# Kernel tuning notes

Hardware: AMD Instinct MI355X
Metric: run time of the kernel (lower is better)

Reference implementation:

```python
import jax, jax.numpy as jnp
import numpy as np

N = 100000      # nodes
E = 1600000     # edges
G = 1024        # graphs in batch
BASE = 1000     # baseline (TF-IDF) dim
AUG = 384       # augmented (LM) dim
H = 256         # hidden dim
C = 2           # classes
EPS = 1e-5      # BatchNorm eps


def setup_inputs() -> dict:
    key = jax.random.key(0)
    ks = jax.random.split(key, 10)
    x = jax.random.normal(ks[0], (N, BASE), jnp.float32)
    x_aug = jax.random.normal(ks[1], (N, AUG), jnp.float32)
    edge_index = jax.random.randint(ks[2], (2, E), 0, N)
    batch = jnp.sort(jax.random.randint(ks[3], (N,), 0, G))

    def lin(k, fin, fout):
        return (jax.random.normal(k, (fin, fout), jnp.float32) / np.sqrt(fin)).astype(jnp.float32)

    return dict(
        x=x, x_aug=x_aug,
        fusion_W=lin(ks[4], BASE + AUG, H), fusion_b=jnp.zeros((H,), jnp.float32),
        W0=lin(ks[5], H, H), b0=jnp.zeros((H,), jnp.float32),
        g0=jnp.ones((H,), jnp.float32), be0=jnp.zeros((H,), jnp.float32),
        W1=lin(ks[6], H, H), b1=jnp.zeros((H,), jnp.float32),
        g1=jnp.ones((H,), jnp.float32), be1=jnp.zeros((H,), jnp.float32),
        fc_W=lin(ks[7], H, C), fc_b=jnp.zeros((C,), jnp.float32),
        edge_index=edge_index, batch=batch,
    )


def _gcn(h, W, b, src, dst, dinv):
    # PyG GCNConv: x' = D^{-1/2}(A+I)D^{-1/2} (x W) + b, self-loop weight 1
    h = h @ W                                     # [N, H]
    norm = dinv[src] * dinv[dst]                  # [E]
    agg = jax.ops.segment_sum(h[src] * norm[:, None], dst, num_segments=N)
    agg = agg + h * (dinv * dinv)[:, None]        # self-loop term
    return agg + b


def _bn(x, gamma, beta):
    # training-mode BatchNorm1d (batch statistics, biased variance)
    m = x.mean(axis=0)
    v = x.var(axis=0)
    return (x - m) * jax.lax.rsqrt(v + EPS) * gamma + beta


def reference(x, x_aug, fusion_W, fusion_b, W0, b0, g0, be0, W1, b1, g1, be1,
              fc_W, fc_b, edge_index, batch):
    src, dst = edge_index[0], edge_index[1]
    # degrees with self-loops (edge weight 1), scattered at destination
    deg = jnp.zeros((N,), x.dtype).at[dst].add(1.0) + 1.0
    dinv = jax.lax.rsqrt(deg)

    # feature fusion ('concat'): Linear(baseline+aug -> hidden) + ReLU
    h = jax.nn.relu(jnp.concatenate([x, x_aug], axis=1) @ fusion_W + fusion_b)

    # GCN layer 1 + BN + ReLU (dropout is identity in eval)
    h = jax.nn.relu(_bn(_gcn(h, W0, b0, src, dst, dinv), g0, be0))
    # GCN layer 2 + BN + ReLU
    h = jax.nn.relu(_bn(_gcn(h, W1, b1, src, dst, dinv), g1, be1))

    # global mean pool over graphs
    cnt = jax.ops.segment_sum(jnp.ones((N,), h.dtype), batch, num_segments=G)
    pooled = jax.ops.segment_sum(h, batch, num_segments=G) / jnp.maximum(cnt, 1.0)[:, None]

    logits = pooled @ fc_W + fc_b                 # [G, C]
    return jax.nn.log_softmax(logits, axis=1)
```

## Files before the change

### kernel.cpp

```cpp
#include <hip/hip_runtime.h>
#include <hip/hip_bf16.h>

#define N_NODES 100000
#define N_EDGES 1600000
#define N_GRAPH 1024
#define DIM_BASE 1000
#define DIM_AUG 384
#define DIM_IN 1384
#define KPAD_IN 1408
#define HD 256
#define BN_EPS 1e-5f

typedef _Float16 f16x8 __attribute__((ext_vector_type(8)));
typedef _Float16 f16x4 __attribute__((ext_vector_type(4)));
typedef float f32x4 __attribute__((ext_vector_type(4)));

__global__ void zero_kernel(unsigned int* __restrict__ p, int n) {
    int i = blockIdx.x * blockDim.x + threadIdx.x;
    if (i < n) p[i] = 0u;
}

__global__ void count_edges_kernel(const int* __restrict__ dst, int* __restrict__ counts, int e) {
    int i = blockIdx.x * blockDim.x + threadIdx.x;
    if (i < e) atomicAdd(&counts[dst[i]], 1);
}

__global__ __launch_bounds__(256) void deg_bsum_kernel(const int* __restrict__ counts,
                                                       int* __restrict__ bsum, int n) {
    __shared__ int sh[256];
    int t = threadIdx.x;
    int base = blockIdx.x * 1024 + t * 4;
    int s = 0;
    if (base < n) {
        int4 v = *(const int4*)&counts[base];
        s = v.x + v.y + v.z + v.w;
    }
    sh[t] = s;
    __syncthreads();
    for (int off = 128; off > 0; off >>= 1) {
        if (t < off) sh[t] += sh[t + off];
        __syncthreads();
    }
    if (t == 0) bsum[blockIdx.x] = sh[0];
}

__global__ __launch_bounds__(128) void scan_bsum_kernel(const int* __restrict__ bsum,
                                                        int* __restrict__ boff, int nb) {
    __shared__ int sh[128];
    int t = threadIdx.x;
    int v = (t < nb) ? bsum[t] : 0;
    sh[t] = v;
    __syncthreads();
    for (int off = 1; off < 128; off <<= 1) {
        int u = (t >= off) ? sh[t - off] : 0;
        __syncthreads();
        sh[t] += u;
        __syncthreads();
    }
    if (t < nb) boff[t] = sh[t] - v;
}

__global__ __launch_bounds__(256) void emit_csr_kernel(const int* __restrict__ counts,
                                                       const int* __restrict__ boff,
                                                       int* __restrict__ row_ptr,
                                                       int* __restrict__ cursor,
                                                       float* __restrict__ dinv, int n, int etot) {
    __shared__ int sh[256];
    int t = threadIdx.x;
    int base = blockIdx.x * 1024 + t * 4;
    int c0 = 0, c1 = 0, c2 = 0, c3 = 0;
    if (base < n) {
        int4 v = *(const int4*)&counts[base];
        c0 = v.x; c1 = v.y; c2 = v.z; c3 = v.w;
    }
    int s = c0 + c1 + c2 + c3;
    sh[t] = s;
    __syncthreads();
    for (int off = 1; off < 256; off <<= 1) {
        int u = (t >= off) ? sh[t - off] : 0;
        __syncthreads();
        sh[t] += u;
        __syncthreads();
    }
    if (base < n) {
        int run = boff[blockIdx.x] + sh[t] - s;
        int4 rp;
        rp.x = run; run += c0;
        rp.y = run; run += c1;
        rp.z = run; run += c2;
        rp.w = run;
        *(int4*)&row_ptr[base] = rp;
        *(int4*)&cursor[base] = rp;
        float4 dv;
        dv.x = rsqrtf((float)c0 + 1.0f);
        dv.y = rsqrtf((float)c1 + 1.0f);
        dv.z = rsqrtf((float)c2 + 1.0f);
        dv.w = rsqrtf((float)c3 + 1.0f);
        *(float4*)&dinv[base] = dv;
    }
    if (blockIdx.x == 0 && t == 0) row_ptr[n] = etot;
}

__global__ void fill_edges_kernel(const int* __restrict__ src, const int* __restrict__ dst,
                                  int* __restrict__ cursor, int* __restrict__ col, int e) {
    int i = blockIdx.x * blockDim.x + threadIdx.x;
    if (i < e) {
        int pos = atomicAdd(&cursor[dst[i]], 1);
        col[pos] = src[i];
    }
}

__global__ __launch_bounds__(256) void btrans_kernel(const float* __restrict__ W,
                                                     f16x8* __restrict__ Bt,
                                                     int K, int nchunks) {
    int idx = blockIdx.x * 256 + threadIdx.x;
    if (idx >= nchunks) return;
    int col = idx & 255;
    int kbase = (idx >> 8) * 8;
    f16x8 h;
#pragma unroll
    for (int j = 0; j < 8; ++j) {
        int k = kbase + j;
        float v = (k < K) ? W[(size_t)k * HD + col] : 0.f;
        h[j] = (_Float16)v;
    }
    Bt[idx] = h;
}

__global__ __launch_bounds__(512, 4) void fusion_mfma_kernel(
        const float* __restrict__ x, const float* __restrict__ xa,
        const f16x8* __restrict__ Bt, const float* __restrict__ bias,
        _Float16* __restrict__ C, int M) {
    __shared__ _Float16 Al[2][128 * 40];
    int tid = threadIdx.x;
    int lane = tid & 63;
    int wid = tid >> 6;
    int wr = wid >> 2, wc = wid & 3;
    int l16 = lane & 15, l4 = lane >> 4;
    int row0 = blockIdx.x * 128;

    f32x4 acc[4][4];
#pragma unroll
    for (int m = 0; m < 4; ++m)
#pragma unroll
        for (int n = 0; n < 4; ++n) acc[m][n] = (f32x4){0.f, 0.f, 0.f, 0.f};

    int arow = tid >> 2;
    int akq = (tid & 3) * 8;
    int ar = row0 + arow;
    int arc = (ar < M) ? ar : (M - 1);

    auto loadA = [&](int s, float* fv) {
        int kg = s * 32 + akq;
        if (kg < DIM_IN) {
            const float* sp = (kg < DIM_BASE) ? (x + (size_t)arc * DIM_BASE + kg)
                                              : (xa + (size_t)arc * DIM_AUG + (kg - DIM_BASE));
            float4 v0 = ((const float4*)sp)[0];
            float4 v1 = ((const float4*)sp)[1];
            fv[0] = v0.x; fv[1] = v0.y; fv[2] = v0.z; fv[3] = v0.w;
            fv[4] = v1.x; fv[5] = v1.y; fv[6] = v1.z; fv[7] = v1.w;
        } else {
#pragma unroll
            for (int j = 0; j < 8; ++j) fv[j] = 0.f;
        }
    };

    const int S = KPAD_IN / 32;
    float fv0[8], fv1[8];
    loadA(0, fv0);
    loadA(1, fv1);

    int bcol = wc * 64 + l16;

    auto iter = [&](int s, float* fv) {
        int buf = s & 1;
        f16x8 av;
#pragma unroll
        for (int j = 0; j < 8; ++j) av[j] = (_Float16)fv[j];
        *(f16x8*)&Al[buf][arow * 40 + akq] = av;
        if (s + 2 < S) loadA(s + 2, fv);
        __syncthreads();
        f16x8 bf[4];
#pragma unroll
        for (int n = 0; n < 4; ++n)
            bf[n] = Bt[(size_t)(s * 4 + l4) * 256 + bcol + n * 16];
#pragma unroll
        for (int m = 0; m < 4; ++m) {
            f16x8 af = *(const f16x8*)&Al[buf][(wr * 64 + m * 16 + l16) * 40 + l4 * 8];
#pragma unroll
            for (int n = 0; n < 4; ++n)
                acc[m][n] = __builtin_amdgcn_mfma_f32_16x16x32_f16(af, bf[n], acc[m][n], 0, 0, 0);
        }
    };

    for (int s = 0; s < S; s += 2) {
        iter(s, fv0);
        iter(s + 1, fv1);
    }

#pragma unroll
    for (int n = 0; n < 4; ++n) {
        int colF = wc * 64 + n * 16 + l16;
        float bc = bias[colF];
#pragma unroll
        for (int m = 0; m < 4; ++m) {
#pragma unroll
            for (int r = 0; r < 4; ++r) {
                int rowF = row0 + wr * 64 + m * 16 + l4 * 4 + r;
                if (rowF < M)
                    C[(size_t)rowF * HD + colF] = (_Float16)fmaxf(acc[m][n][r] + bc, 0.f);
            }
        }
    }
}

__global__ __launch_bounds__(512, 4) void hgemm_f16_kernel(
        const _Float16* __restrict__ A, const f16x8* __restrict__ Bt,
        _Float16* __restrict__ C, int M) {
    __shared__ _Float16 Al[2][128 * 40];
    int tid = threadIdx.x;
    int lane = tid & 63;
    int wid = tid >> 6;
    int wr = wid >> 2, wc = wid & 3;
    int l16 = lane & 15, l4 = lane >> 4;
    int row0 = blockIdx.x * 128;

    f32x4 acc[4][4];
#pragma unroll
    for (int m = 0; m < 4; ++m)
#pragma unroll
        for (int n = 0; n < 4; ++n) acc[m][n] = (f32x4){0.f, 0.f, 0.f, 0.f};

    int arow = tid >> 2;
    int akq = (tid & 3) * 8;
    int ar = row0 + arow;
    int arc = (ar < M) ? ar : (M - 1);
    int bcol = wc * 64 + l16;

    const int S = HD / 32;
    f16x8 av0 = *(const f16x8*)&A[(size_t)arc * HD + akq];
    f16x8 av1 = *(const f16x8*)&A[(size_t)arc * HD + 32 + akq];

    auto iter = [&](int s, f16x8& av) {
        int buf = s & 1;
        *(f16x8*)&Al[buf][arow * 40 + akq] = av;
        if (s + 2 < S) av = *(const f16x8*)&A[(size_t)arc * HD + (s + 2) * 32 + akq];
        __syncthreads();
        f16x8 bf[4];
#pragma unroll
        for (int n = 0; n < 4; ++n)
            bf[n] = Bt[(size_t)(s * 4 + l4) * 256 + bcol + n * 16];
#pragma unroll
        for (int m = 0; m < 4; ++m) {
            f16x8 af = *(const f16x8*)&Al[buf][(wr * 64 + m * 16 + l16) * 40 + l4 * 8];
#pragma unroll
            for (int n = 0; n < 4; ++n)
                acc[m][n] = __builtin_amdgcn_mfma_f32_16x16x32_f16(af, bf[n], acc[m][n], 0, 0, 0);
        }
    };

    for (int s = 0; s < S; s += 2) {
        iter(s, av0);
        iter(s + 1, av1);
    }

#pragma unroll
    for (int n = 0; n < 4; ++n) {
        int colF = wc * 64 + n * 16 + l16;
#pragma unroll
        for (int m = 0; m < 4; ++m) {
#pragma unroll
            for (int r = 0; r < 4; ++r) {
                int rowF = row0 + wr * 64 + m * 16 + l4 * 4 + r;
                if (rowF < M)
                    C[(size_t)rowF * HD + colF] = (_Float16)acc[m][n][r];
            }
        }
    }
}

__global__ __launch_bounds__(512, 4) void hgemm_bn_kernel(
        const float* __restrict__ A, const f16x8* __restrict__ Bt,
        const float* __restrict__ bnp, _Float16* __restrict__ C, int M) {
    __shared__ _Float16 Al[2][128 * 40];
    __shared__ float bns[512];
    int tid = threadIdx.x;
    int lane = tid & 63;
    int wid = tid >> 6;
    int wr = wid >> 2, wc = wid & 3;
    int l16 = lane & 15, l4 = lane >> 4;
    int row0 = blockIdx.x * 128;

    bns[tid] = bnp[tid];
    __syncthreads();

    f32x4 acc[4][4];
#pragma unroll
    for (int m = 0; m < 4; ++m)
#pragma unroll
        for (int n = 0; n < 4; ++n) acc[m][n] = (f32x4){0.f, 0.f, 0.f, 0.f};

    int arow = tid >> 2;
    int akq = (tid & 3) * 8;
    int ar = row0 + arow;
    int arc = (ar < M) ? ar : (M - 1);
    int bcol = wc * 64 + l16;

    auto loadA = [&](int s, float* fv) {
        const float* sp = A + (size_t)arc * HD + s * 32 + akq;
        float4 v0 = ((const float4*)sp)[0];
        float4 v1 = ((const float4*)sp)[1];
        fv[0] = v0.x; fv[1] = v0.y; fv[2] = v0.z; fv[3] = v0.w;
        fv[4] = v1.x; fv[5] = v1.y; fv[6] = v1.z; fv[7] = v1.w;
    };

    const int S = HD / 32;
    float fv0[8], fv1[8];
    loadA(0, fv0);
    loadA(1, fv1);

    auto iter = [&](int s, float* fv) {
        int buf = s & 1;
        int kg = s * 32 + akq;
        f16x8 av;
#pragma unroll
        for (int j = 0; j < 8; ++j)
            av[j] = (_Float16)fmaxf(fmaf(fv[j], bns[kg + j], bns[HD + kg + j]), 0.f);
        *(f16x8*)&Al[buf][arow * 40 + akq] = av;
        if (s + 2 < S) loadA(s + 2, fv);
        __syncthreads();
        f16x8 bf[4];
#pragma unroll
        for (int n = 0; n < 4; ++n)
            bf[n] = Bt[(size_t)(s * 4 + l4) * 256 + bcol + n * 16];
#pragma unroll
        for (int m = 0; m < 4; ++m) {
            f16x8 af = *(const f16x8*)&Al[buf][(wr * 64 + m * 16 + l16) * 40 + l4 * 8];
#pragma unroll
            for (int n = 0; n < 4; ++n)
                acc[m][n] = __builtin_amdgcn_mfma_f32_16x16x32_f16(af, bf[n], acc[m][n], 0, 0, 0);
        }
    };

    for (int s = 0; s < S; s += 2) {
        iter(s, fv0);
        iter(s + 1, fv1);
    }

#pragma unroll
    for (int n = 0; n < 4; ++n) {
        int colF = wc * 64 + n * 16 + l16;
#pragma unroll
        for (int m = 0; m < 4; ++m) {
#pragma unroll
            for (int r = 0; r < 4; ++r) {
                int rowF = row0 + wr * 64 + m * 16 + l4 * 4 + r;
                if (rowF < M)
                    C[(size_t)rowF * HD + colF] = (_Float16)acc[m][n][r];
            }
        }
    }
}

__global__ __launch_bounds__(256) void agg_kernel(
        const _Float16* __restrict__ t, const float* __restrict__ dinv,
        const int* __restrict__ row_ptr, const int* __restrict__ col,
        const float* __restrict__ bias, float* __restrict__ outp, int n) {
    int wid = threadIdx.x >> 6;
    int lane = threadIdx.x & 63;
    int i = blockIdx.x * 4 + wid;
    if (i >= n) return;
    int c0 = lane * 4;
    float di = dinv[i];
    float di2 = di * di;
    f16x4 sv = *(const f16x4*)&t[(size_t)i * HD + c0];
    float a0 = (float)sv[0] * di2, a1 = (float)sv[1] * di2;
    float a2 = (float)sv[2] * di2, a3 = (float)sv[3] * di2;
    int e = row_ptr[i], end = row_ptr[i + 1];
    for (; e + 1 < end; e += 2) {
        int s0 = col[e], s1 = col[e + 1];
        float w0 = dinv[s0] * di, w1 = dinv[s1] * di;
        f16x4 v0 = *(const f16x4*)&t[(size_t)s0 * HD + c0];
        f16x4 v1 = *(const f16x4*)&t[(size_t)s1 * HD + c0];
        a0 = fmaf((float)v0[0], w0, a0); a1 = fmaf((float)v0[1], w0, a1);
        a2 = fmaf((float)v0[2], w0, a2); a3 = fmaf((float)v0[3], w0, a3);
        a0 = fmaf((float)v1[0], w1, a0); a1 = fmaf((float)v1[1], w1, a1);
        a2 = fmaf((float)v1[2], w1, a2); a3 = fmaf((float)v1[3], w1, a3);
    }
    if (e < end) {
        int s0 = col[e];
        float w0 = dinv[s0] * di;
        f16x4 v0 = *(const f16x4*)&t[(size_t)s0 * HD + c0];
        a0 = fmaf((float)v0[0], w0, a0); a1 = fmaf((float)v0[1], w0, a1);
        a2 = fmaf((float)v0[2], w0, a2); a3 = fmaf((float)v0[3], w0, a3);
    }
    float4 b = *(const float4*)&bias[c0];
    float4 o;
    o.x = a0 + b.x; o.y = a1 + b.y; o.z = a2 + b.z; o.w = a3 + b.w;
    *(float4*)&outp[(size_t)i * HD + c0] = o;
}

__global__ __launch_bounds__(256) void bn_stats_kernel(const float* __restrict__ a,
                                                       float* __restrict__ sums, int n) {
    int tid = threadIdx.x;
    int r0 = blockIdx.x * 256;
    int r1 = min(r0 + 256, n);
    float s = 0.f, s2 = 0.f;
    for (int r = r0; r < r1; ++r) {
        float v = a[(size_t)r * HD + tid];
        s += v;
        s2 = fmaf(v, v, s2);
    }
    atomicAdd(&sums[tid], s);
    atomicAdd(&sums[HD + tid], s2);
}

__global__ __launch_bounds__(256) void bn_final_kernel(const float* __restrict__ sums,
                                                       const float* __restrict__ g,
                                                       const float* __restrict__ be,
                                                       float* __restrict__ p, int n) {
    int tid = threadIdx.x;
    float mean = sums[tid] / (float)n;
    float var = sums[HD + tid] / (float)n - mean * mean;
    float sc = g[tid] * rsqrtf(var + BN_EPS);
    p[tid] = sc;
    p[HD + tid] = be[tid] - mean * sc;
}

__global__ void graph_cnt_kernel(const int* __restrict__ batch, float* __restrict__ cnt, int n) {
    int i = blockIdx.x * blockDim.x + threadIdx.x;
    if (i < n) atomicAdd(&cnt[batch[i]], 1.0f);
}

__global__ __launch_bounds__(256) void bn_relu_pool_kernel(const float* __restrict__ a,
                                                           const float* __restrict__ p,
                                                           const int* __restrict__ batch,
                                                           float* __restrict__ pooled, int n) {
    int tid = threadIdx.x;
    int n0 = blockIdx.x * 64;
    int n1 = min(n0 + 64, n);
    if (n0 >= n) return;
    float sc = p[tid], sh = p[HD + tid];
    int curg = batch[n0];
    float acc = 0.f;
    for (int i = n0; i < n1; ++i) {
        int g = batch[i];
        if (g != curg) {
            atomicAdd(&pooled[(size_t)curg * HD + tid], acc);
            acc = 0.f;
            curg = g;
        }
        acc += fmaxf(fmaf(a[(size_t)i * HD + tid], sc, sh), 0.f);
    }
    atomicAdd(&pooled[(size_t)curg * HD + tid], acc);
}

__global__ __launch_bounds__(64) void head_kernel(const float* __restrict__ pooled,
                                                  const float* __restrict__ cnt,
                                                  const float* __restrict__ fcW,
                                                  const float* __restrict__ fcb,
                                                  float* __restrict__ outp) {
    int g = blockIdx.x, lane = threadIdx.x;
    float inv = 1.0f / fmaxf(cnt[g], 1.0f);
    float a0 = 0.f, a1 = 0.f;
    for (int j = lane; j < HD; j += 64) {
        float v = pooled[(size_t)g * HD + j] * inv;
        a0 = fmaf(v, fcW[j * 2 + 0], a0);
        a1 = fmaf(v, fcW[j * 2 + 1], a1);
    }
    for (int off = 32; off > 0; off >>= 1) {
        a0 += __shfl_down(a0, off);
        a1 += __shfl_down(a1, off);
    }
    if (lane == 0) {
        float l0 = a0 + fcb[0], l1 = a1 + fcb[1];
        float m = fmaxf(l0, l1);
        float lse = m + logf(expf(l0 - m) + expf(l1 - m));
        outp[g * 2 + 0] = l0 - lse;
        outp[g * 2 + 1] = l1 - lse;
    }
}

extern "C" void kernel_launch(void* const* d_in, const int* in_sizes, int n_in,
                              void* d_out, int out_size, void* d_ws, size_t ws_size,
                              hipStream_t stream) {
    const float* x        = (const float*)d_in[0];
    const float* x_aug    = (const float*)d_in[1];
    const float* fusion_W = (const float*)d_in[2];
    const float* fusion_b = (const float*)d_in[3];
    const float* W0       = (const float*)d_in[4];
    const float* b0       = (const float*)d_in[5];
    const float* g0       = (const float*)d_in[6];
    const float* be0      = (const float*)d_in[7];
    const float* W1       = (const float*)d_in[8];
    const float* b1       = (const float*)d_in[9];
    const float* g1       = (const float*)d_in[10];
    const float* be1      = (const float*)d_in[11];
    const float* fc_W     = (const float*)d_in[12];
    const float* fc_b     = (const float*)d_in[13];
    const int*   eidx     = (const int*)d_in[14];
    const int*   batch    = (const int*)d_in[15];
    float* outp = (float*)d_out;

    const int N = N_NODES, E = N_EDGES, G = N_GRAPH;
    const int* src = eidx;
    const int* dst = eidx + E;

    size_t off = 0;
    char* ws = (char*)d_ws;
    auto take = [&](size_t nbytes) -> void* {
        void* p = ws + off;
        off = (off + nbytes + 255) & ~(size_t)255;
        return p;
    };
    float*     bufA    = (float*)take((size_t)N * HD * 4);
    _Float16*  bufH    = (_Float16*)take((size_t)N * HD * 2);
    _Float16*  bufT    = (_Float16*)take((size_t)N * HD * 2);
    float*     dinv    = (float*)take((size_t)N * 4);
    int*       row_ptr = (int*)take((size_t)(N + 1) * 4);
    int*       cursor  = (int*)take((size_t)N * 4);
    int*       col     = (int*)take((size_t)E * 4);
    float*     bn1p    = (float*)take(512 * 4);
    float*     bn2p    = (float*)take(512 * 4);
    int*       bsum    = (int*)take(128 * 4);
    int*       boff    = (int*)take(128 * 4);
    f16x8*     BtF     = (f16x8*)take((size_t)(KPAD_IN / 8) * 256 * 16);
    f16x8*     Bt0     = (f16x8*)take((size_t)(HD / 8) * 256 * 16);
    f16x8*     Bt1     = (f16x8*)take((size_t)(HD / 8) * 256 * 16);
    size_t zwords = (size_t)N + 512 + 512 + (size_t)G * HD + G;
    unsigned int* zbase = (unsigned int*)take(zwords * 4);
    int*   counts = (int*)zbase;
    float* bn1s   = (float*)(zbase + N);
    float* bn2s   = bn1s + 512;
    float* pooled = bn2s + 512;
    float* cnt    = pooled + (size_t)G * HD;

    const int nchF = (KPAD_IN / 8) * 256;
    const int nchH = (HD / 8) * 256;
    const int nScanB = (N + 1023) / 1024;

    zero_kernel<<<(int)((zwords + 255) / 256), 256, 0, stream>>>(zbase, (int)zwords);
    count_edges_kernel<<<(E + 255) / 256, 256, 0, stream>>>(dst, counts, E);
    deg_bsum_kernel<<<nScanB, 256, 0, stream>>>(counts, bsum, N);
    scan_bsum_kernel<<<1, 128, 0, stream>>>(bsum, boff, nScanB);
    emit_csr_kernel<<<nScanB, 256, 0, stream>>>(counts, boff, row_ptr, cursor, dinv, N, E);
    fill_edges_kernel<<<(E + 255) / 256, 256, 0, stream>>>(src, dst, cursor, col, E);
    btrans_kernel<<<(nchF + 255) / 256, 256, 0, stream>>>(fusion_W, BtF, DIM_IN, nchF);
    btrans_kernel<<<(nchH + 255) / 256, 256, 0, stream>>>(W0, Bt0, HD, nchH);
    btrans_kernel<<<(nchH + 255) / 256, 256, 0, stream>>>(W1, Bt1, HD, nchH);

    const int gblocks = (N + 127) / 128;
    fusion_mfma_kernel<<<gblocks, 512, 0, stream>>>(x, x_aug, BtF, fusion_b, bufH, N);
    hgemm_f16_kernel<<<gblocks, 512, 0, stream>>>(bufH, Bt0, bufT, N);
    agg_kernel<<<(N + 3) / 4, 256, 0, stream>>>(bufT, dinv, row_ptr, col, b0, bufA, N);
    bn_stats_kernel<<<(N + 255) / 256, 256, 0, stream>>>(bufA, bn1s, N);
    bn_final_kernel<<<1, 256, 0, stream>>>(bn1s, g0, be0, bn1p, N);
    hgemm_bn_kernel<<<gblocks, 512, 0, stream>>>(bufA, Bt1, bn1p, bufT, N);
    agg_kernel<<<(N + 3) / 4, 256, 0, stream>>>(bufT, dinv, row_ptr, col, b1, bufA, N);
    bn_stats_kernel<<<(N + 255) / 256, 256, 0, stream>>>(bufA, bn2s, N);
    bn_final_kernel<<<1, 256, 0, stream>>>(bn2s, g1, be1, bn2p, N);
    graph_cnt_kernel<<<(N + 255) / 256, 256, 0, stream>>>(batch, cnt, N);
    bn_relu_pool_kernel<<<(N + 63) / 64, 256, 0, stream>>>(bufA, bn2p, batch, pooled, N);
    head_kernel<<<G, 64, 0, stream>>>(pooled, cnt, fc_W, fc_b, outp);
}
```

Measured before the change: 1.017 ms.

## Rework dense GEMMs to register-direct 32x32x16 MFMA without LDS staging

All three dense GEMM kernels (fusion, layer-0, layer-1 with fused BN) drop the shared-memory A staging and __syncthreads. Each wave now owns 32 full rows and loads its A fragments straight from global memory into registers. The kernels also switch from 16x16x32 to 32x32x16 MFMA, covering all 256 output columns per wave with 8 accumulators, and use 256-thread blocks. The aim is to remove LDS round-trips and barrier stalls. The cost is much higher register pressure (128 accumulator floats plus double-buffered B fragments), and B is reloaded per wave with less sharing across waves.

```diff
diff --git a/kernel.cpp b/kernel.cpp
--- a/kernel.cpp
+++ b/kernel.cpp
@@ -14,6 +14,7 @@
 typedef _Float16 f16x8 __attribute__((ext_vector_type(8)));
 typedef _Float16 f16x4 __attribute__((ext_vector_type(4)));
 typedef float f32x4 __attribute__((ext_vector_type(4)));
+typedef float f32x16 __attribute__((ext_vector_type(16)));
 
 __global__ void zero_kernel(unsigned int* __restrict__ p, int n) {
     int i = blockIdx.x * blockDim.x + threadIdx.x;
@@ -127,34 +128,31 @@
     Bt[idx] = h;
 }
 
-__global__ __launch_bounds__(512, 4) void fusion_mfma_kernel(
+
+__global__ __launch_bounds__(256, 2) void fusion_mfma_kernel(
         const float* __restrict__ x, const float* __restrict__ xa,
         const f16x8* __restrict__ Bt, const float* __restrict__ bias,
         _Float16* __restrict__ C, int M) {
-    __shared__ _Float16 Al[2][128 * 40];
     int tid = threadIdx.x;
     int lane = tid & 63;
     int wid = tid >> 6;
-    int wr = wid >> 2, wc = wid & 3;
-    int l16 = lane & 15, l4 = lane >> 4;
-    int row0 = blockIdx.x * 128;
-
-    f32x4 acc[4][4];
-#pragma unroll
-    for (int m = 0; m < 4; ++m)
-#pragma unroll
-        for (int n = 0; n < 4; ++n) acc[m][n] = (f32x4){0.f, 0.f, 0.f, 0.f};
-
-    int arow = tid >> 2;
-    int akq = (tid & 3) * 8;
-    int ar = row0 + arow;
-    int arc = (ar < M) ? ar : (M - 1);
+    int l31 = lane & 31;
+    int lhi = lane >> 5;
+    int row = blockIdx.x * 128 + wid * 32 + l31;
+    int rowc = (row < M) ? row : (M - 1);
+    const float* xr = x + (size_t)rowc * DIM_BASE;
+    const float* xar = xa + (size_t)rowc * DIM_AUG;
+
+    f32x16 acc[8];
+#pragma unroll
+    for (int nf = 0; nf < 8; ++nf)
+#pragma unroll
+        for (int e = 0; e < 16; ++e) acc[nf][e] = 0.f;
 
     auto loadA = [&](int s, float* fv) {
-        int kg = s * 32 + akq;
+        int kg = s * 16 + lhi * 8;
         if (kg < DIM_IN) {
-            const float* sp = (kg < DIM_BASE) ? (x + (size_t)arc * DIM_BASE + kg)
-                                              : (xa + (size_t)arc * DIM_AUG + (kg - DIM_BASE));
+            const float* sp = (kg < DIM_BASE) ? (xr + kg) : (xar + (kg - DIM_BASE));
             float4 v0 = ((const float4*)sp)[0];
             float4 v1 = ((const float4*)sp)[1];
             fv[0] = v0.x; fv[1] = v0.y; fv[2] = v0.z; fv[3] = v0.w;
@@ -164,200 +162,188 @@
             for (int j = 0; j < 8; ++j) fv[j] = 0.f;
         }
     };
-
-    const int S = KPAD_IN / 32;
+    auto loadB = [&](int s, f16x8* bq) {
+        const f16x8* bp = Bt + (size_t)(s * 2 + lhi) * 256 + l31;
+#pragma unroll
+        for (int nf = 0; nf < 8; ++nf) bq[nf] = bp[nf * 32];
+    };
+
+    const int S = KPAD_IN / 16;
     float fv0[8], fv1[8];
+    f16x8 bq0[8], bq1[8];
     loadA(0, fv0);
     loadA(1, fv1);
-
-    int bcol = wc * 64 + l16;
-
-    auto iter = [&](int s, float* fv) {
-        int buf = s & 1;
-        f16x8 av;
-#pragma unroll
-        for (int j = 0; j < 8; ++j) av[j] = (_Float16)fv[j];
-        *(f16x8*)&Al[buf][arow * 40 + akq] = av;
-        if (s + 2 < S) loadA(s + 2, fv);
-        __syncthreads();
-        f16x8 bf[4];
-#pragma unroll
-        for (int n = 0; n < 4; ++n)
-            bf[n] = Bt[(size_t)(s * 4 + l4) * 256 + bcol + n * 16];
-#pragma unroll
-        for (int m = 0; m < 4; ++m) {
-            f16x8 af = *(const f16x8*)&Al[buf][(wr * 64 + m * 16 + l16) * 40 + l4 * 8];
-#pragma unroll
-            for (int n = 0; n < 4; ++n)
-                acc[m][n] = __builtin_amdgcn_mfma_f32_16x16x32_f16(af, bf[n], acc[m][n], 0, 0, 0);
+    loadB(0, bq0);
+
+    for (int s = 0; s < S; s += 2) {
+        f16x8 a0;
+#pragma unroll
+        for (int j = 0; j < 8; ++j) a0[j] = (_Float16)fv0[j];
+        if (s + 2 < S) loadA(s + 2, fv0);
+        loadB(s + 1, bq1);
+#pragma unroll
+        for (int nf = 0; nf < 8; ++nf)
+            acc[nf] = __builtin_amdgcn_mfma_f32_32x32x16_f16(a0, bq0[nf], acc[nf], 0, 0, 0);
+
+        f16x8 a1;
+#pragma unroll
+        for (int j = 0; j < 8; ++j) a1[j] = (_Float16)fv1[j];
+        if (s + 3 < S) loadA(s + 3, fv1);
+        if (s + 2 < S) loadB(s + 2, bq0);
+#pragma unroll
+        for (int nf = 0; nf < 8; ++nf)
+            acc[nf] = __builtin_amdgcn_mfma_f32_32x32x16_f16(a1, bq1[nf], acc[nf], 0, 0, 0);
+    }
+
+    int rbase = blockIdx.x * 128 + wid * 32 + 4 * lhi;
+#pragma unroll
+    for (int nf = 0; nf < 8; ++nf) {
+        int colF = nf * 32 + l31;
+        float bc = bias[colF];
+#pragma unroll
+        for (int r = 0; r < 16; ++r) {
+            int rowF = rbase + (r & 3) + 8 * (r >> 2);
+            if (rowF < M)
+                C[(size_t)rowF * HD + colF] = (_Float16)fmaxf(acc[nf][r] + bc, 0.f);
         }
-    };
-
-    for (int s = 0; s < S; s += 2) {
-        iter(s, fv0);
-        iter(s + 1, fv1);
-    }
-
-#pragma unroll
-    for (int n = 0; n < 4; ++n) {
-        int colF = wc * 64 + n * 16 + l16;
-        float bc = bias[colF];
-#pragma unroll
-        for (int m = 0; m < 4; ++m) {
-#pragma unroll
-            for (int r = 0; r < 4; ++r) {
-                int rowF = row0 + wr * 64 + m * 16 + l4 * 4 + r;
-                if (rowF < M)
-                    C[(size_t)rowF * HD + colF] = (_Float16)fmaxf(acc[m][n][r] + bc, 0.f);
-            }
-        }
-    }
-}
-
-__global__ __launch_bounds__(512, 4) void hgemm_f16_kernel(
+    }
+}
+
+__global__ __launch_bounds__(256, 2) void hgemm_f16_kernel(
         const _Float16* __restrict__ A, const f16x8* __restrict__ Bt,
         _Float16* __restrict__ C, int M) {
-    __shared__ _Float16 Al[2][128 * 40];
     int tid = threadIdx.x;
     int lane = tid & 63;
     int wid = tid >> 6;
-    int wr = wid >> 2, wc = wid & 3;
-    int l16 = lane & 15, l4 = lane >> 4;
-    int row0 = blockIdx.x * 128;
-
-    f32x4 acc[4][4];
-#pragma unroll
-    for (int m = 0; m < 4; ++m)
-#pragma unroll
-        for (int n = 0; n < 4; ++n) acc[m][n] = (f32x4){0.f, 0.f, 0.f, 0.f};
-
-    int arow = tid >> 2;
-    int akq = (tid & 3) * 8;
-    int ar = row0 + arow;
-    int arc = (ar < M) ? ar : (M - 1);
-    int bcol = wc * 64 + l16;
-
-    const int S = HD / 32;
-    f16x8 av0 = *(const f16x8*)&A[(size_t)arc * HD + akq];
-    f16x8 av1 = *(const f16x8*)&A[(size_t)arc * HD + 32 + akq];
-
-    auto iter = [&](int s, f16x8& av) {
-        int buf = s & 1;
-        *(f16x8*)&Al[buf][arow * 40 + akq] = av;
-        if (s + 2 < S) av = *(const f16x8*)&A[(size_t)arc * HD + (s + 2) * 32 + akq];
-        __syncthreads();
-        f16x8 bf[4];
-#pragma unroll
-        for (int n = 0; n < 4; ++n)
-            bf[n] = Bt[(size_t)(s * 4 + l4) * 256 + bcol + n * 16];
-#pragma unroll
-        for (int m = 0; m < 4; ++m) {
-            f16x8 af = *(const f16x8*)&Al[buf][(wr * 64 + m * 16 + l16) * 40 + l4 * 8];
-#pragma unroll
-            for (int n = 0; n < 4; ++n)
-                acc[m][n] = __builtin_amdgcn_mfma_f32_16x16x32_f16(af, bf[n], acc[m][n], 0, 0, 0);
+    int l31 = lane & 31;
+    int lhi = lane >> 5;
+    int row = blockIdx.x * 128 + wid * 32 + l31;
+    int rowc = (row < M) ? row : (M - 1);
+    const _Float16* ar = A + (size_t)rowc * HD + lhi * 8;
+
+    f32x16 acc[8];
+#pragma unroll
+    for (int nf = 0; nf < 8; ++nf)
+#pragma unroll
+        for (int e = 0; e < 16; ++e) acc[nf][e] = 0.f;
+
+    auto loadB = [&](int s, f16x8* bq) {
+        const f16x8* bp = Bt + (size_t)(s * 2 + lhi) * 256 + l31;
+#pragma unroll
+        for (int nf = 0; nf < 8; ++nf) bq[nf] = bp[nf * 32];
+    };
+
+    const int S = HD / 16;
+    f16x8 a0 = *(const f16x8*)(ar + 0 * 16);
+    f16x8 a1 = *(const f16x8*)(ar + 1 * 16);
+    f16x8 bq0[8], bq1[8];
+    loadB(0, bq0);
+
+    for (int s = 0; s < S; s += 2) {
+        f16x8 ac = a0;
+        if (s + 2 < S) a0 = *(const f16x8*)(ar + (s + 2) * 16);
+        loadB(s + 1, bq1);
+#pragma unroll
+        for (int nf = 0; nf < 8; ++nf)
+            acc[nf] = __builtin_amdgcn_mfma_f32_32x32x16_f16(ac, bq0[nf], acc[nf], 0, 0, 0);
+
+        f16x8 ad = a1;
+        if (s + 3 < S) a1 = *(const f16x8*)(ar + (s + 3) * 16);
+        if (s + 2 < S) loadB(s + 2, bq0);
+#pragma unroll
+        for (int nf = 0; nf < 8; ++nf)
+            acc[nf] = __builtin_amdgcn_mfma_f32_32x32x16_f16(ad, bq1[nf], acc[nf], 0, 0, 0);
+    }
+
+    int rbase = blockIdx.x * 128 + wid * 32 + 4 * lhi;
+#pragma unroll
+    for (int nf = 0; nf < 8; ++nf) {
+        int colF = nf * 32 + l31;
+#pragma unroll
+        for (int r = 0; r < 16; ++r) {
+            int rowF = rbase + (r & 3) + 8 * (r >> 2);
+            if (rowF < M)
+                C[(size_t)rowF * HD + colF] = (_Float16)acc[nf][r];
         }
-    };
-
-    for (int s = 0; s < S; s += 2) {
-        iter(s, av0);
-        iter(s + 1, av1);
-    }
-
-#pragma unroll
-    for (int n = 0; n < 4; ++n) {
-        int colF = wc * 64 + n * 16 + l16;
-#pragma unroll
-        for (int m = 0; m < 4; ++m) {
-#pragma unroll
-            for (int r = 0; r < 4; ++r) {
-                int rowF = row0 + wr * 64 + m * 16 + l4 * 4 + r;
-                if (rowF < M)
-                    C[(size_t)rowF * HD + colF] = (_Float16)acc[m][n][r];
-            }
-        }
-    }
-}
-
-__global__ __launch_bounds__(512, 4) void hgemm_bn_kernel(
+    }
+}
+
+__global__ __launch_bounds__(256, 2) void hgemm_bn_kernel(
         const float* __restrict__ A, const f16x8* __restrict__ Bt,
         const float* __restrict__ bnp, _Float16* __restrict__ C, int M) {
-    __shared__ _Float16 Al[2][128 * 40];
     __shared__ float bns[512];
     int tid = threadIdx.x;
+    bns[tid] = bnp[tid];
+    bns[256 + tid] = bnp[256 + tid];
+    __syncthreads();
+
     int lane = tid & 63;
     int wid = tid >> 6;
-    int wr = wid >> 2, wc = wid & 3;
-    int l16 = lane & 15, l4 = lane >> 4;
-    int row0 = blockIdx.x * 128;
-
-    bns[tid] = bnp[tid];
-    __syncthreads();
-
-    f32x4 acc[4][4];
-#pragma unroll
-    for (int m = 0; m < 4; ++m)
-#pragma unroll
-        for (int n = 0; n < 4; ++n) acc[m][n] = (f32x4){0.f, 0.f, 0.f, 0.f};
-
-    int arow = tid >> 2;
-    int akq = (tid & 3) * 8;
-    int ar = row0 + arow;
-    int arc = (ar < M) ? ar : (M - 1);
-    int bcol = wc * 64 + l16;
+    int l31 = lane & 31;
+    int lhi = lane >> 5;
+    int row = blockIdx.x * 128 + wid * 32 + l31;
+    int rowc = (row < M) ? row : (M - 1);
+    const float* ar = A + (size_t)rowc * HD + lhi * 8;
+
+    f32x16 acc[8];
+#pragma unroll
+    for (int nf = 0; nf < 8; ++nf)
+#pragma unroll
+        for (int e = 0; e < 16; ++e) acc[nf][e] = 0.f;
 
     auto loadA = [&](int s, float* fv) {
-        const float* sp = A + (size_t)arc * HD + s * 32 + akq;
+        const float* sp = ar + s * 16;
         float4 v0 = ((const float4*)sp)[0];
         float4 v1 = ((const float4*)sp)[1];
         fv[0] = v0.x; fv[1] = v0.y; fv[2] = v0.z; fv[3] = v0.w;
         fv[4] = v1.x; fv[5] = v1.y; fv[6] = v1.z; fv[7] = v1.w;
     };
-
-    const int S = HD / 32;
+    auto loadB = [&](int s, f16x8* bq) {
+        const f16x8* bp = Bt + (size_t)(s * 2 + lhi) * 256 + l31;
+#pragma unroll
+        for (int nf = 0; nf < 8; ++nf) bq[nf] = bp[nf * 32];
+    };
+    auto cvtbn = [&](int s, const float* fv) -> f16x8 {
+        int kg = s * 16 + lhi * 8;
+        f16x8 a;
+#pragma unroll
+        for (int j = 0; j < 8; ++j)
+            a[j] = (_Float16)fmaxf(fmaf(fv[j], bns[kg + j], bns[HD + kg + j]), 0.f);
+        return a;
+    };
+
+    const int S = HD / 16;
     float fv0[8], fv1[8];
+    f16x8 bq0[8], bq1[8];
     loadA(0, fv0);
     loadA(1, fv1);
-
-    auto iter = [&](int s, float* fv) {
-        int buf = s & 1;
-        int kg = s * 32 + akq;
-        f16x8 av;
-#pragma unroll
-        for (int j = 0; j < 8; ++j)
-            av[j] = (_Float16)fmaxf(fmaf(fv[j], bns[kg + j], bns[HD + kg + j]), 0.f);
-        *(f16x8*)&Al[buf][arow * 40 + akq] = av;
-        if (s + 2 < S) loadA(s + 2, fv);
-        __syncthreads();
-        f16x8 bf[4];
-#pragma unroll
-        for (int n = 0; n < 4; ++n)
-            bf[n] = Bt[(size_t)(s * 4 + l4) * 256 + bcol + n * 16];
-#pragma unroll
-        for (int m = 0; m < 4; ++m) {
-            f16x8 af = *(const f16x8*)&Al[buf][(wr * 64 + m * 16 + l16) * 40 + l4 * 8];
-#pragma unroll
-            for (int n = 0; n < 4; ++n)
-                acc[m][n] = __builtin_amdgcn_mfma_f32_16x16x32_f16(af, bf[n], acc[m][n], 0, 0, 0);
-        }
-    };
+    loadB(0, bq0);
 
     for (int s = 0; s < S; s += 2) {
-        iter(s, fv0);
-        iter(s + 1, fv1);
-    }
-
-#pragma unroll
-    for (int n = 0; n < 4; ++n) {
-        int colF = wc * 64 + n * 16 + l16;
-#pragma unroll
-        for (int m = 0; m < 4; ++m) {
-#pragma unroll
-            for (int r = 0; r < 4; ++r) {
-                int rowF = row0 + wr * 64 + m * 16 + l4 * 4 + r;
-                if (rowF < M)
-                    C[(size_t)rowF * HD + colF] = (_Float16)acc[m][n][r];
-            }
+        f16x8 a0 = cvtbn(s, fv0);
+        if (s + 2 < S) loadA(s + 2, fv0);
+        loadB(s + 1, bq1);
+#pragma unroll
+        for (int nf = 0; nf < 8; ++nf)
+            acc[nf] = __builtin_amdgcn_mfma_f32_32x32x16_f16(a0, bq0[nf], acc[nf], 0, 0, 0);
+
+        f16x8 a1 = cvtbn(s + 1, fv1);
+        if (s + 3 < S) loadA(s + 3, fv1);
+        if (s + 2 < S) loadB(s + 2, bq0);
+#pragma unroll
+        for (int nf = 0; nf < 8; ++nf)
+            acc[nf] = __builtin_amdgcn_mfma_f32_32x32x16_f16(a1, bq1[nf], acc[nf], 0, 0, 0);
+    }
+
+    int rbase = blockIdx.x * 128 + wid * 32 + 4 * lhi;
+#pragma unroll
+    for (int nf = 0; nf < 8; ++nf) {
+        int colF = nf * 32 + l31;
+#pragma unroll
+        for (int r = 0; r < 16; ++r) {
+            int rowF = rbase + (r & 3) + 8 * (r >> 2);
+            if (rowF < M)
+                C[(size_t)rowF * HD + colF] = (_Float16)acc[nf][r];
         }
     }
 }
@@ -550,12 +536,12 @@
     btrans_kernel<<<(nchH + 255) / 256, 256, 0, stream>>>(W1, Bt1, HD, nchH);
 
     const int gblocks = (N + 127) / 128;
-    fusion_mfma_kernel<<<gblocks, 512, 0, stream>>>(x, x_aug, BtF, fusion_b, bufH, N);
-    hgemm_f16_kernel<<<gblocks, 512, 0, stream>>>(bufH, Bt0, bufT, N);
+    fusion_mfma_kernel<<<gblocks, 256, 0, stream>>>(x, x_aug, BtF, fusion_b, bufH, N);
+    hgemm_f16_kernel<<<gblocks, 256, 0, stream>>>(bufH, Bt0, bufT, N);
     agg_kernel<<<(N + 3) / 4, 256, 0, stream>>>(bufT, dinv, row_ptr, col, b0, bufA, N);
     bn_stats_kernel<<<(N + 255) / 256, 256, 0, stream>>>(bufA, bn1s, N);
     bn_final_kernel<<<1, 256, 0, stream>>>(bn1s, g0, be0, bn1p, N);
-    hgemm_bn_kernel<<<gblocks, 512, 0, stream>>>(bufA, Bt1, bn1p, bufT, N);
+    hgemm_bn_kernel<<<gblocks, 256, 0, stream>>>(bufA, Bt1, bn1p, bufT, N);
     agg_kernel<<<(N + 3) / 4, 256, 0, stream>>>(bufT, dinv, row_ptr, col, b1, bufA, N);
     bn_stats_kernel<<<(N + 255) / 256, 256, 0, stream>>>(bufA, bn2s, N);
     bn_final_kernel<<<1, 256, 0, stream>>>(bn2s, g1, be1, bn2p, N);
```

Result: slower. 1.155 ms (+13.6%).

## Retile GEMMs to 64-row blocks with custom barrier keeping loads in flight

Applied to the files above, without the earlier changes.

The three MFMA GEMM kernels move from 128-row blocks with 8 waves to 64-row blocks with 4 waves, each wave covering a 64-column slice. The LDS tile drops its row padding (stride 32 instead of 40). A custom barrier waits only on LDS counters, so global loads of the next A and B tiles stay in flight across the barrier. B fragments are prefetched one step ahead, to overlap memory latency with MFMA work and raise occupancy. The unpadded LDS layout may add bank conflicts, and the hand-written waitcnt depends on the compiler inserting vmcnt waits correctly before data is used.

```diff
diff --git a/kernel.cpp b/kernel.cpp
--- a/kernel.cpp
+++ b/kernel.cpp
@@ -14,6 +14,12 @@
 typedef _Float16 f16x8 __attribute__((ext_vector_type(8)));
 typedef _Float16 f16x4 __attribute__((ext_vector_type(4)));
 typedef float f32x4 __attribute__((ext_vector_type(4)));
+
+__device__ __forceinline__ void barrier_keep_vmem() {
+    __builtin_amdgcn_sched_barrier(0);
+    asm volatile("s_waitcnt lgkmcnt(0)\n\ts_barrier" ::: "memory");
+    __builtin_amdgcn_sched_barrier(0);
+}
 
 __global__ void zero_kernel(unsigned int* __restrict__ p, int n) {
     int i = blockIdx.x * blockDim.x + threadIdx.x;
@@ -127,17 +133,24 @@
     Bt[idx] = h;
 }
 
-__global__ __launch_bounds__(512, 4) void fusion_mfma_kernel(
+
+__global__ __launch_bounds__(256, 4) void fusion_mfma_kernel(
         const float* __restrict__ x, const float* __restrict__ xa,
         const f16x8* __restrict__ Bt, const float* __restrict__ bias,
         _Float16* __restrict__ C, int M) {
-    __shared__ _Float16 Al[2][128 * 40];
+    __shared__ __align__(16) _Float16 Al[2][64 * 32];
     int tid = threadIdx.x;
     int lane = tid & 63;
-    int wid = tid >> 6;
-    int wr = wid >> 2, wc = wid & 3;
+    int wc = tid >> 6;
     int l16 = lane & 15, l4 = lane >> 4;
-    int row0 = blockIdx.x * 128;
+    int row0 = blockIdx.x * 64;
+
+    int srow = tid >> 2;
+    int scol = (tid & 3) * 8;
+    int ar = row0 + srow;
+    int arc = (ar < M) ? ar : (M - 1);
+    const float* xr = x + (size_t)arc * DIM_BASE;
+    const float* xar = xa + (size_t)arc * DIM_AUG;
 
     f32x4 acc[4][4];
 #pragma unroll
@@ -145,58 +158,54 @@
 #pragma unroll
         for (int n = 0; n < 4; ++n) acc[m][n] = (f32x4){0.f, 0.f, 0.f, 0.f};
 
-    int arow = tid >> 2;
-    int akq = (tid & 3) * 8;
-    int ar = row0 + arow;
-    int arc = (ar < M) ? ar : (M - 1);
-
-    auto loadA = [&](int s, float* fv) {
-        int kg = s * 32 + akq;
-        if (kg < DIM_IN) {
-            const float* sp = (kg < DIM_BASE) ? (x + (size_t)arc * DIM_BASE + kg)
-                                              : (xa + (size_t)arc * DIM_AUG + (kg - DIM_BASE));
-            float4 v0 = ((const float4*)sp)[0];
-            float4 v1 = ((const float4*)sp)[1];
-            fv[0] = v0.x; fv[1] = v0.y; fv[2] = v0.z; fv[3] = v0.w;
-            fv[4] = v1.x; fv[5] = v1.y; fv[6] = v1.z; fv[7] = v1.w;
-        } else {
-#pragma unroll
-            for (int j = 0; j < 8; ++j) fv[j] = 0.f;
-        }
-    };
-
-    const int S = KPAD_IN / 32;
-    float fv0[8], fv1[8];
-    loadA(0, fv0);
-    loadA(1, fv1);
-
-    int bcol = wc * 64 + l16;
-
-    auto iter = [&](int s, float* fv) {
-        int buf = s & 1;
-        f16x8 av;
-#pragma unroll
-        for (int j = 0; j < 8; ++j) av[j] = (_Float16)fv[j];
-        *(f16x8*)&Al[buf][arow * 40 + akq] = av;
-        if (s + 2 < S) loadA(s + 2, fv);
-        __syncthreads();
-        f16x8 bf[4];
+    float4 fv[2];
+    f16x8 Bq[4];
+
+    auto loadA = [&](int t) {
+        int col0 = t * 32 + scol;
+        if (col0 > 1376) col0 = 1376;
+        const float* sp = (col0 < DIM_BASE) ? (xr + col0) : (xar + (col0 - DIM_BASE));
+        fv[0] = ((const float4*)sp)[0];
+        fv[1] = ((const float4*)sp)[1];
+    };
+    auto cvwr = [&](int buf) {
+        f16x8 h;
+        h[0] = (_Float16)fv[0].x; h[1] = (_Float16)fv[0].y;
+        h[2] = (_Float16)fv[0].z; h[3] = (_Float16)fv[0].w;
+        h[4] = (_Float16)fv[1].x; h[5] = (_Float16)fv[1].y;
+        h[6] = (_Float16)fv[1].z; h[7] = (_Float16)fv[1].w;
+        *(f16x8*)&Al[buf][srow * 32 + scol] = h;
+    };
+    auto loadB = [&](int t) {
 #pragma unroll
         for (int n = 0; n < 4; ++n)
-            bf[n] = Bt[(size_t)(s * 4 + l4) * 256 + bcol + n * 16];
+            Bq[n] = Bt[(size_t)(t * 4 + l4) * 256 + wc * 64 + n * 16 + l16];
+    };
+    auto compute = [&](int buf) {
 #pragma unroll
         for (int m = 0; m < 4; ++m) {
-            f16x8 af = *(const f16x8*)&Al[buf][(wr * 64 + m * 16 + l16) * 40 + l4 * 8];
+            f16x8 af = *(const f16x8*)&Al[buf][(m * 16 + l16) * 32 + l4 * 8];
 #pragma unroll
             for (int n = 0; n < 4; ++n)
-                acc[m][n] = __builtin_amdgcn_mfma_f32_16x16x32_f16(af, bf[n], acc[m][n], 0, 0, 0);
-        }
-    };
-
-    for (int s = 0; s < S; s += 2) {
-        iter(s, fv0);
-        iter(s + 1, fv1);
-    }
+                acc[m][n] = __builtin_amdgcn_mfma_f32_16x16x32_f16(af, Bq[n], acc[m][n], 0, 0, 0);
+        }
+    };
+
+    const int NT = KPAD_IN / 32;
+    loadA(0);
+    cvwr(0);
+    loadA(1);
+    loadB(0);
+    barrier_keep_vmem();
+
+    for (int t = 0; t < NT - 1; ++t) {
+        cvwr((t + 1) & 1);
+        if (t + 2 < NT) loadA(t + 2);
+        compute(t & 1);
+        loadB(t + 1);
+        barrier_keep_vmem();
+    }
+    compute((NT - 1) & 1);
 
 #pragma unroll
     for (int n = 0; n < 4; ++n) {
@@ -206,7 +215,7 @@
         for (int m = 0; m < 4; ++m) {
 #pragma unroll
             for (int r = 0; r < 4; ++r) {
-                int rowF = row0 + wr * 64 + m * 16 + l4 * 4 + r;
+                int rowF = row0 + m * 16 + l4 * 4 + r;
                 if (rowF < M)
                     C[(size_t)rowF * HD + colF] = (_Float16)fmaxf(acc[m][n][r] + bc, 0.f);
             }
@@ -214,16 +223,21 @@
     }
 }
 
-__global__ __launch_bounds__(512, 4) void hgemm_f16_kernel(
+__global__ __launch_bounds__(256, 4) void hgemm_f16_kernel(
         const _Float16* __restrict__ A, const f16x8* __restrict__ Bt,
         _Float16* __restrict__ C, int M) {
-    __shared__ _Float16 Al[2][128 * 40];
+    __shared__ __align__(16) _Float16 Al[2][64 * 32];
     int tid = threadIdx.x;
     int lane = tid & 63;
-    int wid = tid >> 6;
-    int wr = wid >> 2, wc = wid & 3;
+    int wc = tid >> 6;
     int l16 = lane & 15, l4 = lane >> 4;
-    int row0 = blockIdx.x * 128;
+    int row0 = blockIdx.x * 64;
+
+    int srow = tid >> 2;
+    int scol = (tid & 3) * 8;
+    int ar = row0 + srow;
+    int arc = (ar < M) ? ar : (M - 1);
+    const _Float16* arp = A + (size_t)arc * HD + scol;
 
     f32x4 acc[4][4];
 #pragma unroll
@@ -231,38 +245,39 @@
 #pragma unroll
         for (int n = 0; n < 4; ++n) acc[m][n] = (f32x4){0.f, 0.f, 0.f, 0.f};
 
-    int arow = tid >> 2;
-    int akq = (tid & 3) * 8;
-    int ar = row0 + arow;
-    int arc = (ar < M) ? ar : (M - 1);
-    int bcol = wc * 64 + l16;
-
-    const int S = HD / 32;
-    f16x8 av0 = *(const f16x8*)&A[(size_t)arc * HD + akq];
-    f16x8 av1 = *(const f16x8*)&A[(size_t)arc * HD + 32 + akq];
-
-    auto iter = [&](int s, f16x8& av) {
-        int buf = s & 1;
-        *(f16x8*)&Al[buf][arow * 40 + akq] = av;
-        if (s + 2 < S) av = *(const f16x8*)&A[(size_t)arc * HD + (s + 2) * 32 + akq];
-        __syncthreads();
-        f16x8 bf[4];
+    f16x8 sv;
+    f16x8 Bq[4];
+
+    auto loadB = [&](int t) {
 #pragma unroll
         for (int n = 0; n < 4; ++n)
-            bf[n] = Bt[(size_t)(s * 4 + l4) * 256 + bcol + n * 16];
+            Bq[n] = Bt[(size_t)(t * 4 + l4) * 256 + wc * 64 + n * 16 + l16];
+    };
+    auto compute = [&](int buf) {
 #pragma unroll
         for (int m = 0; m < 4; ++m) {
-            f16x8 af = *(const f16x8*)&Al[buf][(wr * 64 + m * 16 + l16) * 40 + l4 * 8];
+            f16x8 af = *(const f16x8*)&Al[buf][(m * 16 + l16) * 32 + l4 * 8];
 #pragma unroll
             for (int n = 0; n < 4; ++n)
-                acc[m][n] = __builtin_amdgcn_mfma_f32_16x16x32_f16(af, bf[n], acc[m][n], 0, 0, 0);
-        }
-    };
-
-    for (int s = 0; s < S; s += 2) {
-        iter(s, av0);
-        iter(s + 1, av1);
-    }
+                acc[m][n] = __builtin_amdgcn_mfma_f32_16x16x32_f16(af, Bq[n], acc[m][n], 0, 0, 0);
+        }
+    };
+
+    const int NT = HD / 32;
+    sv = *(const f16x8*)(arp);
+    *(f16x8*)&Al[0][srow * 32 + scol] = sv;
+    sv = *(const f16x8*)(arp + 32);
+    loadB(0);
+    barrier_keep_vmem();
+
+    for (int t = 0; t < NT - 1; ++t) {
+        *(f16x8*)&Al[(t + 1) & 1][srow * 32 + scol] = sv;
+        if (t + 2 < NT) sv = *(const f16x8*)(arp + (t + 2) * 32);
+        compute(t & 1);
+        loadB(t + 1);
+        barrier_keep_vmem();
+    }
+    compute((NT - 1) & 1);
 
 #pragma unroll
     for (int n = 0; n < 4; ++n) {
@@ -271,7 +286,7 @@
         for (int m = 0; m < 4; ++m) {
 #pragma unroll
             for (int r = 0; r < 4; ++r) {
-                int rowF = row0 + wr * 64 + m * 16 + l4 * 4 + r;
+                int rowF = row0 + m * 16 + l4 * 4 + r;
                 if (rowF < M)
                     C[(size_t)rowF * HD + colF] = (_Float16)acc[m][n][r];
             }
@@ -279,20 +294,22 @@
     }
 }
 
-__global__ __launch_bounds__(512, 4) void hgemm_bn_kernel(
+__global__ __launch_bounds__(256, 4) void hgemm_bn_kernel(
         const float* __restrict__ A, const f16x8* __restrict__ Bt,
         const float* __restrict__ bnp, _Float16* __restrict__ C, int M) {
-    __shared__ _Float16 Al[2][128 * 40];
+    __shared__ __align__(16) _Float16 Al[2][64 * 32];
     __shared__ float bns[512];
     int tid = threadIdx.x;
     int lane = tid & 63;
-    int wid = tid >> 6;
-    int wr = wid >> 2, wc = wid & 3;
+    int wc = tid >> 6;
     int l16 = lane & 15, l4 = lane >> 4;
-    int row0 = blockIdx.x * 128;
-
-    bns[tid] = bnp[tid];
-    __syncthreads();
+    int row0 = blockIdx.x * 64;
+
+    int srow = tid >> 2;
+    int scol = (tid & 3) * 8;
+    int ar = row0 + srow;
+    int arc = (ar < M) ? ar : (M - 1);
+    const float* arp = A + (size_t)arc * HD + scol;
 
     f32x4 acc[4][4];
 #pragma unroll
@@ -300,52 +317,62 @@
 #pragma unroll
         for (int n = 0; n < 4; ++n) acc[m][n] = (f32x4){0.f, 0.f, 0.f, 0.f};
 
-    int arow = tid >> 2;
-    int akq = (tid & 3) * 8;
-    int ar = row0 + arow;
-    int arc = (ar < M) ? ar : (M - 1);
-    int bcol = wc * 64 + l16;
-
-    auto loadA = [&](int s, float* fv) {
-        const float* sp = A + (size_t)arc * HD + s * 32 + akq;
+    float fv0[8], fv1[8];
+    f16x8 Bq[4];
+
+    auto loadA = [&](int t, float* fv) {
+        const float* sp = arp + t * 32;
         float4 v0 = ((const float4*)sp)[0];
         float4 v1 = ((const float4*)sp)[1];
         fv[0] = v0.x; fv[1] = v0.y; fv[2] = v0.z; fv[3] = v0.w;
         fv[4] = v1.x; fv[5] = v1.y; fv[6] = v1.z; fv[7] = v1.w;
     };
-
-    const int S = HD / 32;
-    float fv0[8], fv1[8];
+    auto cvwr = [&](int t, int buf, const float* fv) {
+        int c = t * 32 + scol;
+        f16x8 h;
+#pragma unroll
+        for (int j = 0; j < 8; ++j)
+            h[j] = (_Float16)fmaxf(fmaf(fv[j], bns[c + j], bns[HD + c + j]), 0.f);
+        *(f16x8*)&Al[buf][srow * 32 + scol] = h;
+    };
+    auto loadB = [&](int t) {
+#pragma unroll
+        for (int n = 0; n < 4; ++n)
+            Bq[n] = Bt[(size_t)(t * 4 + l4) * 256 + wc * 64 + n * 16 + l16];
+    };
+    auto compute = [&](int buf) {
+#pragma unroll
+        for (int m = 0; m < 4; ++m) {
+            f16x8 af = *(const f16x8*)&Al[buf][(m * 16 + l16) * 32 + l4 * 8];
+#pragma unroll
+            for (int n = 0; n < 4; ++n)
+                acc[m][n] = __builtin_amdgcn_mfma_f32_16x16x32_f16(af, Bq[n], acc[m][n], 0, 0, 0);
+        }
+    };
+
+    const int NT = HD / 32;
+    bns[tid] = bnp[tid];
+    bns[256 + tid] = bnp[256 + tid];
     loadA(0, fv0);
     loadA(1, fv1);
-
-    auto iter = [&](int s, float* fv) {
-        int buf = s & 1;
-        int kg = s * 32 + akq;
-        f16x8 av;
-#pragma unroll
-        for (int j = 0; j < 8; ++j)
-            av[j] = (_Float16)fmaxf(fmaf(fv[j], bns[kg + j], bns[HD + kg + j]), 0.f);
-        *(f16x8*)&Al[buf][arow * 40 + akq] = av;
-        if (s + 2 < S) loadA(s + 2, fv);
-        __syncthreads();
-        f16x8 bf[4];
-#pragma unroll
-        for (int n = 0; n < 4; ++n)
-            bf[n] = Bt[(size_t)(s * 4 + l4) * 256 + bcol + n * 16];
-#pragma unroll
-        for (int m = 0; m < 4; ++m) {
-            f16x8 af = *(const f16x8*)&Al[buf][(wr * 64 + m * 16 + l16) * 40 + l4 * 8];
-#pragma unroll
-            for (int n = 0; n < 4; ++n)
-                acc[m][n] = __builtin_amdgcn_mfma_f32_16x16x32_f16(af, bf[n], acc[m][n], 0, 0, 0);
-        }
-    };
-
-    for (int s = 0; s < S; s += 2) {
-        iter(s, fv0);
-        iter(s + 1, fv1);
-    }
+    loadB(0);
+    barrier_keep_vmem();
+    cvwr(0, 0, fv0);
+    barrier_keep_vmem();
+
+    for (int t = 0; t < NT - 1; ++t) {
+        if ((t & 1) == 0) {
+            cvwr(t + 1, (t + 1) & 1, fv1);
+            if (t + 2 < NT) loadA(t + 2, fv0);
+        } else {
+            cvwr(t + 1, (t + 1) & 1, fv0);
+            if (t + 2 < NT) loadA(t + 2, fv1);
+        }
+        compute(t & 1);
+        loadB(t + 1);
+        barrier_keep_vmem();
+    }
+    compute((NT - 1) & 1);
 
 #pragma unroll
     for (int n = 0; n < 4; ++n) {
@@ -354,7 +381,7 @@
         for (int m = 0; m < 4; ++m) {
 #pragma unroll
             for (int r = 0; r < 4; ++r) {
-                int rowF = row0 + wr * 64 + m * 16 + l4 * 4 + r;
+                int rowF = row0 + m * 16 + l4 * 4 + r;
                 if (rowF < M)
                     C[(size_t)rowF * HD + colF] = (_Float16)acc[m][n][r];
             }
@@ -549,13 +576,13 @@
     btrans_kernel<<<(nchH + 255) / 256, 256, 0, stream>>>(W0, Bt0, HD, nchH);
     btrans_kernel<<<(nchH + 255) / 256, 256, 0, stream>>>(W1, Bt1, HD, nchH);
 
-    const int gblocks = (N + 127) / 128;
-    fusion_mfma_kernel<<<gblocks, 512, 0, stream>>>(x, x_aug, BtF, fusion_b, bufH, N);
-    hgemm_f16_kernel<<<gblocks, 512, 0, stream>>>(bufH, Bt0, bufT, N);
+    const int gblocks = (N + 63) / 64;
+    fusion_mfma_kernel<<<gblocks, 256, 0, stream>>>(x, x_aug, BtF, fusion_b, bufH, N);
+    hgemm_f16_kernel<<<gblocks, 256, 0, stream>>>(bufH, Bt0, bufT, N);
     agg_kernel<<<(N + 3) / 4, 256, 0, stream>>>(bufT, dinv, row_ptr, col, b0, bufA, N);
     bn_stats_kernel<<<(N + 255) / 256, 256, 0, stream>>>(bufA, bn1s, N);
     bn_final_kernel<<<1, 256, 0, stream>>>(bn1s, g0, be0, bn1p, N);
-    hgemm_bn_kernel<<<gblocks, 512, 0, stream>>>(bufA, Bt1, bn1p, bufT, N);
+    hgemm_bn_kernel<<<gblocks, 256, 0, stream>>>(bufA, Bt1, bn1p, bufT, N);
     agg_kernel<<<(N + 3) / 4, 256, 0, stream>>>(bufT, dinv, row_ptr, col, b1, bufA, N);
     bn_stats_kernel<<<(N + 255) / 256, 256, 0, stream>>>(bufA, bn2s, N);
     bn_final_kernel<<<1, 256, 0, stream>>>(bn2s, g1, be1, bn2p, N);
```

Measured after the change: 972.8 us. -4.3%, faster.
